# Optimization experiments

Measured on AMD Instinct MI355X. Metric: run time of the kernel, lower is better.

## Reference

```python
import jax, jax.numpy as jnp
import numpy as np

N_NODES = 200000
N_EDGES = 600000
IN_DIM = 130   # hidden_dim + 2
HID = 128
BN_EPS = 1e-5


def setup_inputs() -> dict:
    key = jax.random.key(0)
    ks = jax.random.split(key, 12)
    s = 0.05
    inp = {
        'x': jax.random.normal(ks[0], (N_NODES, IN_DIM), dtype=jnp.float32),
        'edge_index': jax.random.randint(ks[1], (2, N_EDGES), 0, N_NODES, dtype=jnp.int32),
        # SAGEConv 1: lin_l (aggregated neighbors, with bias), lin_r (root, no bias)
        'W1_l': jax.random.normal(ks[2], (IN_DIM, HID), dtype=jnp.float32) * s,
        'b1_l': jnp.zeros((HID,), dtype=jnp.float32),
        'W1_r': jax.random.normal(ks[3], (IN_DIM, HID), dtype=jnp.float32) * s,
        # BatchNorm1d(128) params + running stats (eval mode)
        'g1': jnp.ones((HID,), dtype=jnp.float32),
        'be1': jnp.zeros((HID,), dtype=jnp.float32),
        'rm1': jax.random.normal(ks[4], (HID,), dtype=jnp.float32) * 0.01,
        'rv1': jnp.ones((HID,), dtype=jnp.float32),
        # SAGEConv 2
        'W2_l': jax.random.normal(ks[5], (HID, HID), dtype=jnp.float32) * s,
        'b2_l': jnp.zeros((HID,), dtype=jnp.float32),
        'W2_r': jax.random.normal(ks[6], (HID, HID), dtype=jnp.float32) * s,
        'g2': jnp.ones((HID,), dtype=jnp.float32),
        'be2': jnp.zeros((HID,), dtype=jnp.float32),
        'rm2': jax.random.normal(ks[7], (HID,), dtype=jnp.float32) * 0.01,
        'rv2': jnp.ones((HID,), dtype=jnp.float32),
    }
    return inp


def _sage_mean(x, src, dst, W_l, b_l, W_r, n_nodes):
    # PyG SAGEConv (mean aggr): out = lin_l(mean_{j in N(i)} x_j) + lin_r(x_i)
    msg = x[src]                                                 # [E, F] gather
    agg = jax.ops.segment_sum(msg, dst, num_segments=n_nodes)    # [N, F]
    deg = jax.ops.segment_sum(jnp.ones((src.shape[0], 1), x.dtype), dst,
                              num_segments=n_nodes)              # [N, 1]
    mean = agg / jnp.maximum(deg, 1.0)
    return mean @ W_l + b_l + x @ W_r


def _bn_eval(x, g, b, rm, rv):
    return (x - rm) * (g * jax.lax.rsqrt(rv + BN_EPS)) + b


def reference(x, edge_index, W1_l, b1_l, W1_r, g1, be1, rm1, rv1,
              W2_l, b2_l, W2_r, g2, be2, rm2, rv2):
    src, dst = edge_index[0], edge_index[1]
    n = x.shape[0]
    h = _sage_mean(x, src, dst, W1_l, b1_l, W1_r, n)
    h = jax.nn.relu(_bn_eval(h, g1, be1, rm1, rv1))
    # dropout is identity in eval mode
    h = _sage_mean(h, src, dst, W2_l, b2_l, W2_r, n)
    h = jax.nn.relu(_bn_eval(h, g2, be2, rm2, rv2))
    return h
```

## Files before the change

kernel.cpp:

```cpp
#include <hip/hip_runtime.h>

typedef short v8s __attribute__((ext_vector_type(8)));
typedef float v4f __attribute__((ext_vector_type(4)));
typedef unsigned short v4us __attribute__((ext_vector_type(4)));

__device__ __forceinline__ unsigned short f2bf(float x) {
  union { float f; unsigned int u; } c; c.f = x;
  unsigned int u = c.u;
  return (unsigned short)((u + 0x7fffu + ((u >> 16) & 1u)) >> 16);
}
__device__ __forceinline__ float bf2f(unsigned int hi16) {
  union { unsigned int u; float f; } c; c.u = hi16 << 16;
  return c.f;
}
__device__ __forceinline__ ushort2 pk(float2 v) {
  ushort2 p; p.x = f2bf(v.x); p.y = f2bf(v.y); return p;
}

__device__ __forceinline__ void pack_dev(const float* __restrict__ W,
                                         unsigned short* __restrict__ wpk,
                                         int K, int tot, int i) {
  if (i >= tot) return;
  const int kk = i & 31, n = (i >> 5) & 127, kc = i >> 12;
  const int k = kc * 32 + kk;
  wpk[i] = (k < K) ? f2bf(W[k * 128 + n]) : (unsigned short)0;
}

__global__ void setup_k(const float* __restrict__ g1, const float* __restrict__ be1,
                        const float* __restrict__ rm1, const float* __restrict__ rv1,
                        const float* __restrict__ b1,
                        const float* __restrict__ g2, const float* __restrict__ be2,
                        const float* __restrict__ rm2, const float* __restrict__ rv2,
                        const float* __restrict__ b2,
                        const float* __restrict__ W1l, const float* __restrict__ W1r,
                        const float* __restrict__ W2l, const float* __restrict__ W2r,
                        float* __restrict__ s1, float* __restrict__ t1,
                        float* __restrict__ s2, float* __restrict__ t2,
                        unsigned short* __restrict__ wp1l, unsigned short* __restrict__ wp1r,
                        unsigned short* __restrict__ wp2l, unsigned short* __restrict__ wp2r,
                        unsigned short* __restrict__ bufA, int* __restrict__ degi,
                        int N, int NZB) {
  const int b = blockIdx.x, tid = threadIdx.x;
  if (b < NZB) {
    const int i = b * 256 + tid;
    if (i < N) degi[i] = 0;
    return;
  }
  int r = b - NZB;
  if (r < 80)  { pack_dev(W1l, wp1l, 130, 5 * 4096, r * 256 + tid); return; }
  r -= 80;
  if (r < 80)  { pack_dev(W1r, wp1r, 130, 5 * 4096, r * 256 + tid); return; }
  r -= 80;
  if (r < 64)  { pack_dev(W2l, wp2l, 128, 4 * 4096, r * 256 + tid); return; }
  r -= 64;
  if (r < 64)  { pack_dev(W2r, wp2r, 128, 4 * 4096, r * 256 + tid); return; }
  if (tid < 128) {
    float sv = g1[tid] * rsqrtf(rv1[tid] + 1e-5f);
    s1[tid] = sv; t1[tid] = (b1[tid] - rm1[tid]) * sv + be1[tid];
    float sw = g2[tid] * rsqrtf(rv2[tid] + 1e-5f);
    s2[tid] = sw; t2[tid] = (b2[tid] - rm2[tid]) * sw + be2[tid];
  }
  if (tid < 64) ((unsigned int*)(bufA + (long)N * 128))[tid] = 0u;
}

__global__ __launch_bounds__(256) void scan1_k(const int* __restrict__ degi,
                                               int* __restrict__ rowptr,
                                               int* __restrict__ bsum, int N) {
  __shared__ int sd[256];
  const int t = threadIdx.x;
  const int base = blockIdx.x * 1024 + t * 4;
  int v[4];
#pragma unroll
  for (int j = 0; j < 4; ++j) v[j] = (base + j < N) ? degi[base + j] : 0;
  const int tot = v[0] + v[1] + v[2] + v[3];
  sd[t] = tot;
  __syncthreads();
  for (int off = 1; off < 256; off <<= 1) {
    int o = (t >= off) ? sd[t - off] : 0;
    __syncthreads();
    sd[t] += o;
    __syncthreads();
  }
  int e = sd[t] - tot;
#pragma unroll
  for (int j = 0; j < 4; ++j) {
    if (base + j < N) rowptr[base + j] = e;
    e += v[j];
  }
  if (t == 255) bsum[blockIdx.x] = sd[255];
}
__global__ __launch_bounds__(256) void scan2_k(int* __restrict__ bsum, int nb) {
  __shared__ int sd[256];
  const int t = threadIdx.x;
  const int v = (t < nb) ? bsum[t] : 0;
  sd[t] = v;
  __syncthreads();
  for (int off = 1; off < 256; off <<= 1) {
    int o = (t >= off) ? sd[t - off] : 0;
    __syncthreads();
    sd[t] += o;
    __syncthreads();
  }
  if (t < nb) bsum[t] = sd[t] - v;
}
__global__ void scan3_k(int* __restrict__ rowptr, int* __restrict__ cursor,
                        const int* __restrict__ bsum, int N, int E) {
  int i = blockIdx.x * 256 + threadIdx.x;
  if (i < N) {
    int v = rowptr[i] + bsum[i >> 10];
    rowptr[i] = v;
    cursor[i] = v;
  } else if (i == N) {
    rowptr[N] = E;
  }
}
__global__ void fill_k(const int* __restrict__ src, const int* __restrict__ dst,
                       int* __restrict__ cursor, int* __restrict__ nbr, int E) {
  int i = blockIdx.x * 256 + threadIdx.x;
  if (i < E) {
    int p = atomicAdd(&cursor[dst[i]], 1);
    nbr[p] = src[i];
  }
}

__global__ __launch_bounds__(256) void gemmc_k(const float* __restrict__ Asrc,
                                               const unsigned short* __restrict__ wpk,
                                               unsigned short* __restrict__ O,
                                               const int* __restrict__ dst,
                                               int* __restrict__ degi,
                                               int N, int E, int ngb) {
  constexpr int KC = 5;
  constexpr int KP = KC * 32;
  constexpr int LDA = KP + 8;
  __shared__ __align__(16) unsigned short a_s[64][LDA];
  const int tid = threadIdx.x;

  if ((int)blockIdx.x >= ngb) {
    const int i = ((int)blockIdx.x - ngb) * 256 + tid;
    if (i < E) atomicAdd(&degi[dst[i]], 1);
    return;
  }

  const int node0 = blockIdx.x * 64;
  {
    const int zr = tid >> 2, zq = tid & 3;
    v8s z = {0, 0, 0, 0, 0, 0, 0, 0};
    *(v8s*)&a_s[zr][136 + zq * 8] = z;
    if (tid < 192) {
      const int r3 = tid / 3, p3 = tid - 3 * r3;
      *(unsigned int*)&a_s[r3][130 + 2 * p3] = 0u;
    }
  }
  const float* xb = Asrc + (long)node0 * 130;
  if (node0 + 64 <= N) {
    float4 v[9];
#pragma unroll
    for (int i = 0; i < 9; ++i) {
      const int g = i * 256 + tid;
      if (g < 2080) v[i] = *(const float4*)(xb + 4 * g);
    }
#pragma unroll
    for (int i = 0; i < 9; ++i) {
      const int g = i * 256 + tid;
      if (g < 2080) {
        const int p0 = 2 * g, p1 = 2 * g + 1;
        const int r0_ = (p0 * 4033) >> 18, r1_ = (p1 * 4033) >> 18;
        const int c0_ = p0 - 65 * r0_, c1_ = p1 - 65 * r1_;
        *(ushort2*)&a_s[r0_][2 * c0_] = pk(make_float2(v[i].x, v[i].y));
        *(ushort2*)&a_s[r1_][2 * c1_] = pk(make_float2(v[i].z, v[i].w));
      }
    }
  } else {
    for (int i = 0; i < 9; ++i) {
      const int g = i * 256 + tid;
      if (g < 2080) {
#pragma unroll
        for (int h = 0; h < 2; ++h) {
          const int p = 2 * g + h;
          const int r = (p * 4033) >> 18;
          const int c = p - 65 * r;
          float2 vv = make_float2(0.f, 0.f);
          if (node0 + r < N)
            vv = *(const float2*)(Asrc + (long)(node0 + r) * 130 + 2 * c);
          *(ushort2*)&a_s[r][2 * c] = pk(vv);
        }
      }
    }
  }
  __syncthreads();

  const int wave = tid >> 6, lane = tid & 63;
  const int quad = lane >> 4, l16 = lane & 15;
  v4f acc[4][2];
#pragma unroll
  for (int mt = 0; mt < 4; ++mt)
#pragma unroll
    for (int nt = 0; nt < 2; ++nt) acc[mt][nt] = (v4f){0.f, 0.f, 0.f, 0.f};

  const unsigned short* wb = wpk + (wave * 32 + l16) * 32 + quad * 8;
#pragma unroll
  for (int kc = 0; kc < KC; ++kc) {
    v8s wf[2];
#pragma unroll
    for (int nt = 0; nt < 2; ++nt)
      wf[nt] = *(const v8s*)(wb + kc * 4096 + nt * 512);
#pragma unroll
    for (int mt = 0; mt < 4; ++mt) {
      v8s nf = *(const v8s*)(&a_s[mt * 16 + l16][kc * 32 + quad * 8]);
#pragma unroll
      for (int nt = 0; nt < 2; ++nt)
        acc[mt][nt] = __builtin_amdgcn_mfma_f32_16x16x32_bf16(wf[nt], nf, acc[mt][nt], 0, 0, 0);
    }
  }

#pragma unroll
  for (int mt = 0; mt < 4; ++mt) {
    const int rw = node0 + mt * 16 + l16;
    if (rw < N) {
#pragma unroll
      for (int nt = 0; nt < 2; ++nt) {
        const int oc = wave * 32 + nt * 16 + quad * 4;
        v4us v;
        v[0] = f2bf(acc[mt][nt][0]);
        v[1] = f2bf(acc[mt][nt][1]);
        v[2] = f2bf(acc[mt][nt][2]);
        v[3] = f2bf(acc[mt][nt][3]);
        *(v4us*)(O + (long)rw * 128 + oc) = v;
      }
    }
  }
}

template<int KC>
__global__ __launch_bounds__(256) void gemmB_k(const unsigned short* __restrict__ Asrc,
                                               const unsigned short* __restrict__ wpk,
                                               unsigned short* __restrict__ O, int N) {
  constexpr int KP = KC * 32;
  constexpr int LDA = KP + 8;
  __shared__ __align__(16) unsigned short a_s[64][LDA];
  const int tid = threadIdx.x;
  const int node0 = blockIdx.x * 64;

  const unsigned short* hb = Asrc + (long)node0 * 128;
  v8s v[KC];
#pragma unroll
  for (int i = 0; i < KC; ++i) {
    const int u = i * 256 + tid;
    const int r = u >> 4;
    v[i] = (v8s){0, 0, 0, 0, 0, 0, 0, 0};
    if (node0 + r < N) v[i] = *(const v8s*)(hb + 8 * u);
  }
#pragma unroll
  for (int i = 0; i < KC; ++i) {
    const int u = i * 256 + tid;
    *(v8s*)&a_s[u >> 4][(u & 15) * 8] = v[i];
  }
  __syncthreads();

  const int wave = tid >> 6, lane = tid & 63;
  const int quad = lane >> 4, l16 = lane & 15;
  v4f acc[4][2];
#pragma unroll
  for (int mt = 0; mt < 4; ++mt)
#pragma unroll
    for (int nt = 0; nt < 2; ++nt) acc[mt][nt] = (v4f){0.f, 0.f, 0.f, 0.f};

  const unsigned short* wb = wpk + (wave * 32 + l16) * 32 + quad * 8;
#pragma unroll
  for (int kc = 0; kc < KC; ++kc) {
    v8s wf[2];
#pragma unroll
    for (int nt = 0; nt < 2; ++nt)
      wf[nt] = *(const v8s*)(wb + kc * 4096 + nt * 512);
#pragma unroll
    for (int mt = 0; mt < 4; ++mt) {
      v8s nf = *(const v8s*)(&a_s[mt * 16 + l16][kc * 32 + quad * 8]);
#pragma unroll
      for (int nt = 0; nt < 2; ++nt)
        acc[mt][nt] = __builtin_amdgcn_mfma_f32_16x16x32_bf16(wf[nt], nf, acc[mt][nt], 0, 0, 0);
    }
  }

#pragma unroll
  for (int mt = 0; mt < 4; ++mt) {
    const int rw = node0 + mt * 16 + l16;
    if (rw < N) {
#pragma unroll
      for (int nt = 0; nt < 2; ++nt) {
        const int oc = wave * 32 + nt * 16 + quad * 4;
        v4us v;
        v[0] = f2bf(acc[mt][nt][0]);
        v[1] = f2bf(acc[mt][nt][1]);
        v[2] = f2bf(acc[mt][nt][2]);
        v[3] = f2bf(acc[mt][nt][3]);
        *(v4us*)(O + (long)rw * 128 + oc) = v;
      }
    }
  }
}

template<int KC, bool SRCF32, bool OUTF32>
__global__ __launch_bounds__(256) void spmmR_k(const unsigned short* __restrict__ gsrc,
                                               const void* __restrict__ rsrc,
                                               const unsigned short* __restrict__ wpkr,
                                               const int* __restrict__ rowptr,
                                               const int* __restrict__ nbr,
                                               const float* __restrict__ sc,
                                               const float* __restrict__ tc,
                                               void* __restrict__ out, int N, int E) {
  constexpr int LXS = SRCF32 ? 168 : 136;
  __shared__ __align__(16) unsigned short xls[16][LXS];
  __shared__ __align__(16) float rls[16][132];
  const int tid = threadIdx.x;
  const int lane = tid & 63;
  const int wu = __builtin_amdgcn_readfirstlane(tid >> 6);
  const int quad = lane >> 4, l16 = lane & 15;
  const int nb0 = blockIdx.x * 16;

  if constexpr (SRCF32) {
    {
      if (tid < 64) {
        v8s z = {0, 0, 0, 0, 0, 0, 0, 0};
        *(v8s*)&xls[tid >> 2][136 + (tid & 3) * 8] = z;
      }
      if (tid < 48) {
        const int r3 = tid / 3, p3 = tid - 3 * r3;
        *(unsigned int*)&xls[r3][130 + 2 * p3] = 0u;
      }
    }
    const float* xb = (const float*)rsrc + (long)nb0 * 130;
    if (nb0 + 16 <= N) {
      float4 v[3];
#pragma unroll
      for (int i = 0; i < 3; ++i) {
        const int g = i * 256 + tid;
        if (g < 520) v[i] = *(const float4*)(xb + 4 * g);
      }
#pragma unroll
      for (int i = 0; i < 3; ++i) {
        const int g = i * 256 + tid;
        if (g < 520) {
          const int p0 = 2 * g, p1 = 2 * g + 1;
          const int r0_ = (p0 * 4033) >> 18, r1_ = (p1 * 4033) >> 18;
          const int c0_ = p0 - 65 * r0_, c1_ = p1 - 65 * r1_;
          *(ushort2*)&xls[r0_][2 * c0_] = pk(make_float2(v[i].x, v[i].y));
          *(ushort2*)&xls[r1_][2 * c1_] = pk(make_float2(v[i].z, v[i].w));
        }
      }
    } else {
      for (int i = 0; i < 3; ++i) {
        const int g = i * 256 + tid;
        if (g < 520) {
#pragma unroll
          for (int h = 0; h < 2; ++h) {
            const int p = 2 * g + h;
            const int r = (p * 4033) >> 18;
            const int c = p - 65 * r;
            float2 vv = make_float2(0.f, 0.f);
            if (nb0 + r < N)
              vv = *(const float2*)((const float*)rsrc + (long)(nb0 + r) * 130 + 2 * c);
            *(ushort2*)&xls[r][2 * c] = pk(vv);
          }
        }
      }
    }
  } else {
    const unsigned short* hb = (const unsigned short*)rsrc + (long)nb0 * 128;
    const int r = tid >> 4, c = (tid & 15) * 8;
    v8s v = {0, 0, 0, 0, 0, 0, 0, 0};
    if (nb0 + r < N) v = *(const v8s*)(hb + (long)r * 128 + c);
    *(v8s*)&xls[r][c] = v;
  }

  const int nb = nb0 + wu * 4;
  int r0[4], d[4];
#pragma unroll
  for (int r = 0; r < 4; ++r) {
    const int i0 = min(nb + r, N);
    const int i1 = min(nb + r + 1, N);
    r0[r] = rowptr[i0];
    const int r1 = rowptr[i1];
    d[r] = (nb + r < N) ? (r1 - r0[r]) : 0;
  }
  const int dm = max(max(d[0], d[1]), max(d[2], d[3]));
  float2 a[4];
#pragma unroll
  for (int r = 0; r < 4; ++r) a[r] = make_float2(0.f, 0.f);

  __syncthreads();

  {
    v4f racc[2];
    racc[0] = (v4f){0.f, 0.f, 0.f, 0.f};
    racc[1] = (v4f){0.f, 0.f, 0.f, 0.f};
    const unsigned short* wb = wpkr + (wu * 32 + l16) * 32 + quad * 8;
#pragma unroll
    for (int kc = 0; kc < KC; ++kc) {
      v8s nf = *(const v8s*)&xls[l16][kc * 32 + quad * 8];
#pragma unroll
      for (int nt = 0; nt < 2; ++nt) {
        v8s wf = *(const v8s*)(wb + kc * 4096 + nt * 512);
        racc[nt] = __builtin_amdgcn_mfma_f32_16x16x32_bf16(wf, nf, racc[nt], 0, 0, 0);
      }
    }
#pragma unroll
    for (int nt = 0; nt < 2; ++nt)
      *(v4f*)&rls[l16][wu * 32 + nt * 16 + quad * 4] = racc[nt];
  }

  const int lofs = lane << 1;
  for (int e0 = 0; e0 < dm; e0 += 8) {
    unsigned int u[4][8];
#pragma unroll
    for (int j = 0; j < 8; ++j)
#pragma unroll
      for (int r = 0; r < 4; ++r) {
        const int e = e0 + j;
        const int nv = nbr[min(r0[r] + e, E - 1)];
        const int idx = (e < d[r]) ? nv : N;
        u[r][j] = *(const unsigned int*)(gsrc + ((long)idx << 7) + lofs);
      }
#pragma unroll
    for (int r = 0; r < 4; ++r)
#pragma unroll
      for (int j = 0; j < 8; ++j) {
        a[r].x += bf2f(u[r][j] & 0xffffu);
        a[r].y += bf2f(u[r][j] >> 16);
      }
  }

  __syncthreads();

  const float2 sv = *(const float2*)(sc + 2 * lane);
  const float2 tv = *(const float2*)(tc + 2 * lane);
#pragma unroll
  for (int r = 0; r < 4; ++r) {
    if (nb + r < N) {
      const float inv = 1.0f / fmaxf((float)d[r], 1.0f);
      const float2 rt = *(const float2*)&rls[wu * 4 + r][2 * lane];
      float yx = a[r].x * inv + rt.x;
      float yy = a[r].y * inv + rt.y;
      yx = fmaxf(yx * sv.x + tv.x, 0.f);
      yy = fmaxf(yy * sv.y + tv.y, 0.f);
      if (OUTF32) {
        *(float2*)((float*)out + (long)(nb + r) * 128 + 2 * lane) = make_float2(yx, yy);
      } else {
        *(ushort2*)((unsigned short*)out + (long)(nb + r) * 128 + 2 * lane) =
            pk(make_float2(yx, yy));
      }
    }
  }
}

extern "C" void kernel_launch(void* const* d_in, const int* in_sizes, int n_in,
                              void* d_out, int out_size, void* d_ws, size_t ws_size,
                              hipStream_t stream) {
  const float* x   = (const float*)d_in[0];
  const int*   ei  = (const int*)d_in[1];
  const float* W1l = (const float*)d_in[2];
  const float* b1  = (const float*)d_in[3];
  const float* W1r = (const float*)d_in[4];
  const float* g1  = (const float*)d_in[5];
  const float* be1 = (const float*)d_in[6];
  const float* rm1 = (const float*)d_in[7];
  const float* rv1 = (const float*)d_in[8];
  const float* W2l = (const float*)d_in[9];
  const float* b2  = (const float*)d_in[10];
  const float* W2r = (const float*)d_in[11];
  const float* g2  = (const float*)d_in[12];
  const float* be2 = (const float*)d_in[13];
  const float* rm2 = (const float*)d_in[14];
  const float* rv2 = (const float*)d_in[15];

  const int E = in_sizes[1] / 2;
  const int N = in_sizes[0] / 130;
  const int* src = ei;
  const int* dst = ei + E;

  unsigned short* bufA = (unsigned short*)d_ws;
  unsigned short* bufB = bufA + (size_t)(N + 1) * 128;
  unsigned short* wp1l = bufB + (size_t)(N + 1) * 128;
  unsigned short* wp1r = wp1l + 5 * 4096;
  unsigned short* wp2l = wp1r + 5 * 4096;
  unsigned short* wp2r = wp2l + 4 * 4096;
  float* s1 = (float*)(wp2r + 4 * 4096);
  float* t1 = s1 + 128;
  float* s2 = t1 + 128;
  float* t2 = s2 + 128;
  int* degi   = (int*)(t2 + 128);
  int* rowptr = degi + N;
  int* bsum   = rowptr + N + 1;
  int* nbr    = bsum + 256;

  const int NZB = (N + 255) / 256;
  const int ngb = (N + 63) / 64;
  const int ecb = (E + 255) / 256;
  const int nsb = (N + 15) / 16;

  hipLaunchKernelGGL(setup_k, dim3(NZB + 288 + 1), dim3(256), 0, stream,
                     g1, be1, rm1, rv1, b1, g2, be2, rm2, rv2, b2,
                     W1l, W1r, W2l, W2r, s1, t1, s2, t2,
                     wp1l, wp1r, wp2l, wp2r, bufA, degi, N, NZB);

  hipLaunchKernelGGL(gemmc_k, dim3(ngb + ecb), dim3(256), 0, stream,
                     x, wp1l, bufA, dst, degi, N, E, ngb);

  const int nb = (N + 1023) / 1024;
  hipLaunchKernelGGL(scan1_k, dim3(nb), dim3(256), 0, stream, degi, rowptr, bsum, N);
  hipLaunchKernelGGL(scan2_k, dim3(1), dim3(256), 0, stream, bsum, nb);
  hipLaunchKernelGGL(scan3_k, dim3((N + 256) / 256), dim3(256), 0, stream,
                     rowptr, degi, bsum, N, E);
  hipLaunchKernelGGL(fill_k, dim3(ecb), dim3(256), 0, stream,
                     src, dst, degi, nbr, E);

  hipLaunchKernelGGL((spmmR_k<5, true, false>), dim3(nsb), dim3(256), 0, stream,
                     bufA, (const void*)x, wp1r, rowptr, nbr, s1, t1, (void*)bufB, N, E);
  hipLaunchKernelGGL((gemmB_k<4>), dim3(ngb), dim3(256), 0, stream,
                     bufB, wp2l, bufA, N);
  hipLaunchKernelGGL((spmmR_k<4, false, true>), dim3(nsb), dim3(256), 0, stream,
                     bufA, (const void*)bufB, wp2r, rowptr, nbr, s2, t2, d_out, N, E);
}
```

Baseline: 416.7 us.

## Compute neighbor and root projections in one concatenated-weight GEMM per layer

Both weight matrices of each SAGE layer are packed into one 256-column bf16 block, so the dense GEMM kernels emit both the neighbor projection and the root projection in a single pass. The SpMM kernels no longer stage the root rows in LDS or run their own MFMA; they only gather and average the precomputed neighbor projections and add the stored root term. The separate block-sum scan kernel is folded into scan3, where each block reduces the needed prefix itself, and the bf16 unpack in the gather loop is simplified. In exchange there is an extra N×128 bf16 buffer with its own write and read, and the layer-1 root term is now rounded to bf16 before being added.

```diff
diff --git a/kernel.cpp b/kernel.cpp
--- a/kernel.cpp
+++ b/kernel.cpp
@@ -9,21 +9,26 @@
   unsigned int u = c.u;
   return (unsigned short)((u + 0x7fffu + ((u >> 16) & 1u)) >> 16);
 }
-__device__ __forceinline__ float bf2f(unsigned int hi16) {
-  union { unsigned int u; float f; } c; c.u = hi16 << 16;
-  return c.f;
+__device__ __forceinline__ float bflo(unsigned int u) {
+  union { unsigned int u; float f; } c; c.u = u << 16; return c.f;
+}
+__device__ __forceinline__ float bfhi(unsigned int u) {
+  union { unsigned int u; float f; } c; c.u = u & 0xffff0000u; return c.f;
 }
 __device__ __forceinline__ ushort2 pk(float2 v) {
   ushort2 p; p.x = f2bf(v.x); p.y = f2bf(v.y); return p;
 }
 
-__device__ __forceinline__ void pack_dev(const float* __restrict__ W,
-                                         unsigned short* __restrict__ wpk,
-                                         int K, int tot, int i) {
+__device__ __forceinline__ void pack2_dev(const float* __restrict__ Wl,
+                                          const float* __restrict__ Wr,
+                                          unsigned short* __restrict__ wpk,
+                                          int K, int tot, int i) {
   if (i >= tot) return;
-  const int kk = i & 31, n = (i >> 5) & 127, kc = i >> 12;
+  const int kk = i & 31, n = (i >> 5) & 255, kc = i >> 13;
   const int k = kc * 32 + kk;
-  wpk[i] = (k < K) ? f2bf(W[k * 128 + n]) : (unsigned short)0;
+  float v = 0.f;
+  if (k < K) v = (n < 128) ? Wl[k * 128 + n] : Wr[k * 128 + (n - 128)];
+  wpk[i] = f2bf(v);
 }
 
 __global__ void setup_k(const float* __restrict__ g1, const float* __restrict__ be1,
@@ -36,8 +41,7 @@
                         const float* __restrict__ W2l, const float* __restrict__ W2r,
                         float* __restrict__ s1, float* __restrict__ t1,
                         float* __restrict__ s2, float* __restrict__ t2,
-                        unsigned short* __restrict__ wp1l, unsigned short* __restrict__ wp1r,
-                        unsigned short* __restrict__ wp2l, unsigned short* __restrict__ wp2r,
+                        unsigned short* __restrict__ wp1, unsigned short* __restrict__ wp2,
                         unsigned short* __restrict__ bufA, int* __restrict__ degi,
                         int N, int NZB) {
   const int b = blockIdx.x, tid = threadIdx.x;
@@ -47,13 +51,9 @@
     return;
   }
   int r = b - NZB;
-  if (r < 80)  { pack_dev(W1l, wp1l, 130, 5 * 4096, r * 256 + tid); return; }
-  r -= 80;
-  if (r < 80)  { pack_dev(W1r, wp1r, 130, 5 * 4096, r * 256 + tid); return; }
-  r -= 80;
-  if (r < 64)  { pack_dev(W2l, wp2l, 128, 4 * 4096, r * 256 + tid); return; }
-  r -= 64;
-  if (r < 64)  { pack_dev(W2r, wp2r, 128, 4 * 4096, r * 256 + tid); return; }
+  if (r < 160) { pack2_dev(W1l, W1r, wp1, 130, 5 * 8192, r * 256 + tid); return; }
+  r -= 160;
+  if (r < 128) { pack2_dev(W2l, W2r, wp2, 128, 4 * 8192, r * 256 + tid); return; }
   if (tid < 128) {
     float sv = g1[tid] * rsqrtf(rv1[tid] + 1e-5f);
     s1[tid] = sv; t1[tid] = (b1[tid] - rm1[tid]) * sv + be1[tid];
@@ -89,25 +89,23 @@
   }
   if (t == 255) bsum[blockIdx.x] = sd[255];
 }
-__global__ __launch_bounds__(256) void scan2_k(int* __restrict__ bsum, int nb) {
+__global__ __launch_bounds__(256) void scan3_k(int* __restrict__ rowptr,
+                                               int* __restrict__ cursor,
+                                               const int* __restrict__ bsum,
+                                               int N, int E) {
   __shared__ int sd[256];
   const int t = threadIdx.x;
-  const int v = (t < nb) ? bsum[t] : 0;
-  sd[t] = v;
+  const int chunk = blockIdx.x >> 2;
+  sd[t] = (t < chunk) ? bsum[t] : 0;
   __syncthreads();
-  for (int off = 1; off < 256; off <<= 1) {
-    int o = (t >= off) ? sd[t - off] : 0;
+  for (int off = 128; off >= 1; off >>= 1) {
+    if (t < off) sd[t] += sd[t + off];
     __syncthreads();
-    sd[t] += o;
-    __syncthreads();
-  }
-  if (t < nb) bsum[t] = sd[t] - v;
-}
-__global__ void scan3_k(int* __restrict__ rowptr, int* __restrict__ cursor,
-                        const int* __restrict__ bsum, int N, int E) {
-  int i = blockIdx.x * 256 + threadIdx.x;
+  }
+  const int S = sd[0];
+  const int i = blockIdx.x * 256 + t;
   if (i < N) {
-    int v = rowptr[i] + bsum[i >> 10];
+    const int v = rowptr[i] + S;
     rowptr[i] = v;
     cursor[i] = v;
   } else if (i == N) {
@@ -125,7 +123,8 @@
 
 __global__ __launch_bounds__(256) void gemmc_k(const float* __restrict__ Asrc,
                                                const unsigned short* __restrict__ wpk,
-                                               unsigned short* __restrict__ O,
+                                               unsigned short* __restrict__ Ol,
+                                               unsigned short* __restrict__ Or,
                                                const int* __restrict__ dst,
                                                int* __restrict__ degi,
                                                int N, int E, int ngb) {
@@ -191,50 +190,53 @@
 
   const int wave = tid >> 6, lane = tid & 63;
   const int quad = lane >> 4, l16 = lane & 15;
-  v4f acc[4][2];
+  v4f acc[4][4];
 #pragma unroll
   for (int mt = 0; mt < 4; ++mt)
 #pragma unroll
-    for (int nt = 0; nt < 2; ++nt) acc[mt][nt] = (v4f){0.f, 0.f, 0.f, 0.f};
-
-  const unsigned short* wb = wpk + (wave * 32 + l16) * 32 + quad * 8;
+    for (int nt = 0; nt < 4; ++nt) acc[mt][nt] = (v4f){0.f, 0.f, 0.f, 0.f};
+
+  const unsigned short* wb = wpk + (wave * 64 + l16) * 32 + quad * 8;
 #pragma unroll
   for (int kc = 0; kc < KC; ++kc) {
-    v8s wf[2];
-#pragma unroll
-    for (int nt = 0; nt < 2; ++nt)
-      wf[nt] = *(const v8s*)(wb + kc * 4096 + nt * 512);
+    v8s wf[4];
+#pragma unroll
+    for (int nt = 0; nt < 4; ++nt)
+      wf[nt] = *(const v8s*)(wb + kc * 8192 + nt * 512);
 #pragma unroll
     for (int mt = 0; mt < 4; ++mt) {
       v8s nf = *(const v8s*)(&a_s[mt * 16 + l16][kc * 32 + quad * 8]);
 #pragma unroll
-      for (int nt = 0; nt < 2; ++nt)
+      for (int nt = 0; nt < 4; ++nt)
         acc[mt][nt] = __builtin_amdgcn_mfma_f32_16x16x32_bf16(wf[nt], nf, acc[mt][nt], 0, 0, 0);
     }
   }
 
+  unsigned short* ob = (wave < 2) ? Ol : Or;
+  const int cb = (wave & 1) * 64;
 #pragma unroll
   for (int mt = 0; mt < 4; ++mt) {
     const int rw = node0 + mt * 16 + l16;
     if (rw < N) {
 #pragma unroll
-      for (int nt = 0; nt < 2; ++nt) {
-        const int oc = wave * 32 + nt * 16 + quad * 4;
+      for (int nt = 0; nt < 4; ++nt) {
+        const int oc = cb + nt * 16 + quad * 4;
         v4us v;
         v[0] = f2bf(acc[mt][nt][0]);
         v[1] = f2bf(acc[mt][nt][1]);
         v[2] = f2bf(acc[mt][nt][2]);
         v[3] = f2bf(acc[mt][nt][3]);
-        *(v4us*)(O + (long)rw * 128 + oc) = v;
-      }
-    }
-  }
-}
-
-template<int KC>
+        *(v4us*)(ob + (long)rw * 128 + oc) = v;
+      }
+    }
+  }
+}
+
 __global__ __launch_bounds__(256) void gemmB_k(const unsigned short* __restrict__ Asrc,
                                                const unsigned short* __restrict__ wpk,
-                                               unsigned short* __restrict__ O, int N) {
+                                               unsigned short* __restrict__ Ol,
+                                               unsigned short* __restrict__ Or, int N) {
+  constexpr int KC = 4;
   constexpr int KP = KC * 32;
   constexpr int LDA = KP + 8;
   __shared__ __align__(16) unsigned short a_s[64][LDA];
@@ -259,120 +261,61 @@
 
   const int wave = tid >> 6, lane = tid & 63;
   const int quad = lane >> 4, l16 = lane & 15;
-  v4f acc[4][2];
+  v4f acc[4][4];
 #pragma unroll
   for (int mt = 0; mt < 4; ++mt)
 #pragma unroll
-    for (int nt = 0; nt < 2; ++nt) acc[mt][nt] = (v4f){0.f, 0.f, 0.f, 0.f};
-
-  const unsigned short* wb = wpk + (wave * 32 + l16) * 32 + quad * 8;
+    for (int nt = 0; nt < 4; ++nt) acc[mt][nt] = (v4f){0.f, 0.f, 0.f, 0.f};
+
+  const unsigned short* wb = wpk + (wave * 64 + l16) * 32 + quad * 8;
 #pragma unroll
   for (int kc = 0; kc < KC; ++kc) {
-    v8s wf[2];
-#pragma unroll
-    for (int nt = 0; nt < 2; ++nt)
-      wf[nt] = *(const v8s*)(wb + kc * 4096 + nt * 512);
+    v8s wf[4];
+#pragma unroll
+    for (int nt = 0; nt < 4; ++nt)
+      wf[nt] = *(const v8s*)(wb + kc * 8192 + nt * 512);
 #pragma unroll
     for (int mt = 0; mt < 4; ++mt) {
       v8s nf = *(const v8s*)(&a_s[mt * 16 + l16][kc * 32 + quad * 8]);
 #pragma unroll
-      for (int nt = 0; nt < 2; ++nt)
+      for (int nt = 0; nt < 4; ++nt)
         acc[mt][nt] = __builtin_amdgcn_mfma_f32_16x16x32_bf16(wf[nt], nf, acc[mt][nt], 0, 0, 0);
     }
   }
 
+  unsigned short* ob = (wave < 2) ? Ol : Or;
+  const int cb = (wave & 1) * 64;
 #pragma unroll
   for (int mt = 0; mt < 4; ++mt) {
     const int rw = node0 + mt * 16 + l16;
     if (rw < N) {
 #pragma unroll
-      for (int nt = 0; nt < 2; ++nt) {
-        const int oc = wave * 32 + nt * 16 + quad * 4;
+      for (int nt = 0; nt < 4; ++nt) {
+        const int oc = cb + nt * 16 + quad * 4;
         v4us v;
         v[0] = f2bf(acc[mt][nt][0]);
         v[1] = f2bf(acc[mt][nt][1]);
         v[2] = f2bf(acc[mt][nt][2]);
         v[3] = f2bf(acc[mt][nt][3]);
-        *(v4us*)(O + (long)rw * 128 + oc) = v;
-      }
-    }
-  }
-}
-
-template<int KC, bool SRCF32, bool OUTF32>
-__global__ __launch_bounds__(256) void spmmR_k(const unsigned short* __restrict__ gsrc,
-                                               const void* __restrict__ rsrc,
-                                               const unsigned short* __restrict__ wpkr,
+        *(v4us*)(ob + (long)rw * 128 + oc) = v;
+      }
+    }
+  }
+}
+
+template<bool OUTF32>
+__global__ __launch_bounds__(256) void spmmL_k(const unsigned short* __restrict__ gsrc,
+                                               const unsigned short* __restrict__ rsrc,
                                                const int* __restrict__ rowptr,
                                                const int* __restrict__ nbr,
                                                const float* __restrict__ sc,
                                                const float* __restrict__ tc,
                                                void* __restrict__ out, int N, int E) {
-  constexpr int LXS = SRCF32 ? 168 : 136;
-  __shared__ __align__(16) unsigned short xls[16][LXS];
-  __shared__ __align__(16) float rls[16][132];
   const int tid = threadIdx.x;
   const int lane = tid & 63;
   const int wu = __builtin_amdgcn_readfirstlane(tid >> 6);
-  const int quad = lane >> 4, l16 = lane & 15;
-  const int nb0 = blockIdx.x * 16;
-
-  if constexpr (SRCF32) {
-    {
-      if (tid < 64) {
-        v8s z = {0, 0, 0, 0, 0, 0, 0, 0};
-        *(v8s*)&xls[tid >> 2][136 + (tid & 3) * 8] = z;
-      }
-      if (tid < 48) {
-        const int r3 = tid / 3, p3 = tid - 3 * r3;
-        *(unsigned int*)&xls[r3][130 + 2 * p3] = 0u;
-      }
-    }
-    const float* xb = (const float*)rsrc + (long)nb0 * 130;
-    if (nb0 + 16 <= N) {
-      float4 v[3];
-#pragma unroll
-      for (int i = 0; i < 3; ++i) {
-        const int g = i * 256 + tid;
-        if (g < 520) v[i] = *(const float4*)(xb + 4 * g);
-      }
-#pragma unroll
-      for (int i = 0; i < 3; ++i) {
-        const int g = i * 256 + tid;
-        if (g < 520) {
-          const int p0 = 2 * g, p1 = 2 * g + 1;
-          const int r0_ = (p0 * 4033) >> 18, r1_ = (p1 * 4033) >> 18;
-          const int c0_ = p0 - 65 * r0_, c1_ = p1 - 65 * r1_;
-          *(ushort2*)&xls[r0_][2 * c0_] = pk(make_float2(v[i].x, v[i].y));
-          *(ushort2*)&xls[r1_][2 * c1_] = pk(make_float2(v[i].z, v[i].w));
-        }
-      }
-    } else {
-      for (int i = 0; i < 3; ++i) {
-        const int g = i * 256 + tid;
-        if (g < 520) {
-#pragma unroll
-          for (int h = 0; h < 2; ++h) {
-            const int p = 2 * g + h;
-            const int r = (p * 4033) >> 18;
-            const int c = p - 65 * r;
-            float2 vv = make_float2(0.f, 0.f);
-            if (nb0 + r < N)
-              vv = *(const float2*)((const float*)rsrc + (long)(nb0 + r) * 130 + 2 * c);
-            *(ushort2*)&xls[r][2 * c] = pk(vv);
-          }
-        }
-      }
-    }
-  } else {
-    const unsigned short* hb = (const unsigned short*)rsrc + (long)nb0 * 128;
-    const int r = tid >> 4, c = (tid & 15) * 8;
-    v8s v = {0, 0, 0, 0, 0, 0, 0, 0};
-    if (nb0 + r < N) v = *(const v8s*)(hb + (long)r * 128 + c);
-    *(v8s*)&xls[r][c] = v;
-  }
-
-  const int nb = nb0 + wu * 4;
+  const int nb = blockIdx.x * 16 + wu * 4;
+
   int r0[4], d[4];
 #pragma unroll
   for (int r = 0; r < 4; ++r) {
@@ -387,27 +330,6 @@
 #pragma unroll
   for (int r = 0; r < 4; ++r) a[r] = make_float2(0.f, 0.f);
 
-  __syncthreads();
-
-  {
-    v4f racc[2];
-    racc[0] = (v4f){0.f, 0.f, 0.f, 0.f};
-    racc[1] = (v4f){0.f, 0.f, 0.f, 0.f};
-    const unsigned short* wb = wpkr + (wu * 32 + l16) * 32 + quad * 8;
-#pragma unroll
-    for (int kc = 0; kc < KC; ++kc) {
-      v8s nf = *(const v8s*)&xls[l16][kc * 32 + quad * 8];
-#pragma unroll
-      for (int nt = 0; nt < 2; ++nt) {
-        v8s wf = *(const v8s*)(wb + kc * 4096 + nt * 512);
-        racc[nt] = __builtin_amdgcn_mfma_f32_16x16x32_bf16(wf, nf, racc[nt], 0, 0, 0);
-      }
-    }
-#pragma unroll
-    for (int nt = 0; nt < 2; ++nt)
-      *(v4f*)&rls[l16][wu * 32 + nt * 16 + quad * 4] = racc[nt];
-  }
-
   const int lofs = lane << 1;
   for (int e0 = 0; e0 < dm; e0 += 8) {
     unsigned int u[4][8];
@@ -424,12 +346,10 @@
     for (int r = 0; r < 4; ++r)
 #pragma unroll
       for (int j = 0; j < 8; ++j) {
-        a[r].x += bf2f(u[r][j] & 0xffffu);
-        a[r].y += bf2f(u[r][j] >> 16);
-      }
-  }
-
-  __syncthreads();
+        a[r].x += bflo(u[r][j]);
+        a[r].y += bfhi(u[r][j]);
+      }
+  }
 
   const float2 sv = *(const float2*)(sc + 2 * lane);
   const float2 tv = *(const float2*)(tc + 2 * lane);
@@ -437,11 +357,9 @@
   for (int r = 0; r < 4; ++r) {
     if (nb + r < N) {
       const float inv = 1.0f / fmaxf((float)d[r], 1.0f);
-      const float2 rt = *(const float2*)&rls[wu * 4 + r][2 * lane];
-      float yx = a[r].x * inv + rt.x;
-      float yy = a[r].y * inv + rt.y;
-      yx = fmaxf(yx * sv.x + tv.x, 0.f);
-      yy = fmaxf(yy * sv.y + tv.y, 0.f);
+      const unsigned int ur = *(const unsigned int*)(rsrc + ((long)(nb + r) << 7) + lofs);
+      float yx = fmaxf((a[r].x * inv + bflo(ur)) * sv.x + tv.x, 0.f);
+      float yy = fmaxf((a[r].y * inv + bfhi(ur)) * sv.y + tv.y, 0.f);
       if (OUTF32) {
         *(float2*)((float*)out + (long)(nb + r) * 128 + 2 * lane) = make_float2(yx, yy);
       } else {
@@ -479,11 +397,10 @@
 
   unsigned short* bufA = (unsigned short*)d_ws;
   unsigned short* bufB = bufA + (size_t)(N + 1) * 128;
-  unsigned short* wp1l = bufB + (size_t)(N + 1) * 128;
-  unsigned short* wp1r = wp1l + 5 * 4096;
-  unsigned short* wp2l = wp1r + 5 * 4096;
-  unsigned short* wp2r = wp2l + 4 * 4096;
-  float* s1 = (float*)(wp2r + 4 * 4096);
+  unsigned short* bufC = bufB + (size_t)(N + 1) * 128;
+  unsigned short* wp1  = bufC + (size_t)N * 128;
+  unsigned short* wp2  = wp1 + 5 * 8192;
+  float* s1 = (float*)(wp2 + 4 * 8192);
   float* t1 = s1 + 128;
   float* s2 = t1 + 128;
   float* t2 = s2 + 128;
@@ -496,27 +413,26 @@
   const int ngb = (N + 63) / 64;
   const int ecb = (E + 255) / 256;
   const int nsb = (N + 15) / 16;
+  const int nb1k = (N + 1023) / 1024;
 
   hipLaunchKernelGGL(setup_k, dim3(NZB + 288 + 1), dim3(256), 0, stream,
                      g1, be1, rm1, rv1, b1, g2, be2, rm2, rv2, b2,
                      W1l, W1r, W2l, W2r, s1, t1, s2, t2,
-                     wp1l, wp1r, wp2l, wp2r, bufA, degi, N, NZB);
+                     wp1, wp2, bufA, degi, N, NZB);
 
   hipLaunchKernelGGL(gemmc_k, dim3(ngb + ecb), dim3(256), 0, stream,
-                     x, wp1l, bufA, dst, degi, N, E, ngb);
-
-  const int nb = (N + 1023) / 1024;
-  hipLaunchKernelGGL(scan1_k, dim3(nb), dim3(256), 0, stream, degi, rowptr, bsum, N);
-  hipLaunchKernelGGL(scan2_k, dim3(1), dim3(256), 0, stream, bsum, nb);
+                     x, wp1, bufA, bufB, dst, degi, N, E, ngb);
+
+  hipLaunchKernelGGL(scan1_k, dim3(nb1k), dim3(256), 0, stream, degi, rowptr, bsum, N);
   hipLaunchKernelGGL(scan3_k, dim3((N + 256) / 256), dim3(256), 0, stream,
                      rowptr, degi, bsum, N, E);
   hipLaunchKernelGGL(fill_k, dim3(ecb), dim3(256), 0, stream,
                      src, dst, degi, nbr, E);
 
-  hipLaunchKernelGGL((spmmR_k<5, true, false>), dim3(nsb), dim3(256), 0, stream,
-                     bufA, (const void*)x, wp1r, rowptr, nbr, s1, t1, (void*)bufB, N, E);
-  hipLaunchKernelGGL((gemmB_k<4>), dim3(ngb), dim3(256), 0, stream,
-                     bufB, wp2l, bufA, N);
-  hipLaunchKernelGGL((spmmR_k<4, false, true>), dim3(nsb), dim3(256), 0, stream,
-                     bufA, (const void*)bufB, wp2r, rowptr, nbr, s2, t2, d_out, N, E);
-}
+  hipLaunchKernelGGL((spmmL_k<false>), dim3(nsb), dim3(256), 0, stream,
+                     bufA, bufB, rowptr, nbr, s1, t1, (void*)bufB, N, E);
+  hipLaunchKernelGGL(gemmB_k, dim3(ngb), dim3(256), 0, stream,
+                     bufB, wp2, bufA, bufC, N);
+  hipLaunchKernelGGL((spmmL_k<true>), dim3(nsb), dim3(256), 0, stream,
+                     bufA, bufC, rowptr, nbr, s2, t2, d_out, N, E);
+}
```

Measured after the change: 420.2 us. No clear change (+0.8%).
